# Kernel optimization log

Hardware: AMD Instinct MI355X
Metric: run time of the kernel (lower is better)

## Reference

```python
import jax, jax.numpy as jnp
import numpy as np

N_HEADS = 4
HEAD_DIM = 6
D_MODEL = 24


def setup_inputs() -> dict:
    key = jax.random.key(0)
    ks = jax.random.split(key, 7)
    B, Tq, Tk = 16, 1024, 1024
    X = jax.random.normal(ks[0], (B, Tq, D_MODEL), dtype=jnp.float32)
    X_en = jax.random.normal(ks[1], (B, Tk, D_MODEL), dtype=jnp.float32)
    I_m = jax.random.randint(ks[2], (B, Tq, Tk), 0, 2, dtype=jnp.int32)
    scale = 1.0 / np.sqrt(D_MODEL)
    Wq = jax.random.normal(ks[3], (D_MODEL, D_MODEL), dtype=jnp.float32) * scale
    Wk = jax.random.normal(ks[4], (D_MODEL, D_MODEL), dtype=jnp.float32) * scale
    Wv = jax.random.normal(ks[5], (D_MODEL, D_MODEL), dtype=jnp.float32) * scale
    Wo = jax.random.normal(ks[6], (D_MODEL, D_MODEL), dtype=jnp.float32) * scale
    return {"X": X, "X_en": X_en, "I_m": I_m, "Wq": Wq, "Wk": Wk, "Wv": Wv, "Wo": Wo}


def _split_heads(x):
    # [B, T, 24] -> [B, 4, T, 6]
    B, T, _ = x.shape
    return x.reshape(B, T, N_HEADS, HEAD_DIM).transpose(0, 2, 1, 3)


def reference(X, X_en, I_m, Wq, Wk, Wv, Wo):
    # torch Linear (no bias): x @ W.T
    Q = _split_heads(X @ Wq.T)      # [B, H, Tq, d]
    K = _split_heads(X_en @ Wk.T)   # [B, H, Tk, d]
    V = _split_heads(X_en @ Wv.T)   # [B, H, Tk, d]
    scale = 1.0 / jnp.sqrt(jnp.asarray(HEAD_DIM, dtype=Q.dtype))
    A = jnp.einsum('bhqd,bhkd->bhqk', Q, K) * scale
    # NOTE: the original torch code calls A.masked_fill(...) without assigning
    # the result, so the mask I_m has NO effect. Faithfully reproduced here.
    A = jax.nn.softmax(A, axis=-1)
    O = jnp.einsum('bhqk,bhkd->bhqd', A, V)  # [B, H, Tq, d]
    B, H, Tq, d = O.shape
    O = O.transpose(0, 2, 1, 3).reshape(B, Tq, H * d)  # [B, Tq, 24]
    return O @ Wo.T
```

## Files before the change

kernel.cpp:

```cpp
#include <hip/hip_runtime.h>
#include <hip/hip_bf16.h>

#define NB 16
#define TT 1024
#define NH 4
#define HD 6
#define DM 24

#define QSC 0.5889785f
#define MBIAS 32.0f

typedef float v2f __attribute__((ext_vector_type(2)));
typedef short bf16x8 __attribute__((ext_vector_type(8)));
typedef float f32x16 __attribute__((ext_vector_type(16)));
typedef unsigned u32x2 __attribute__((ext_vector_type(2)));

__device__ __forceinline__ unsigned cvt_pk_bf16(float lo, float hi) {
  unsigned r;
  asm("v_cvt_pk_bf16_f32 %0, %1, %2" : "=v"(r) : "v"(lo), "v"(hi));
  return r;
}

__device__ __forceinline__ bf16x8 as_bf16x8(uint4 u) {
  union { uint4 u; bf16x8 b; } c;
  c.u = u;
  return c.b;
}

__device__ __forceinline__ float dot24(const float4* r,
                                       const float* __restrict__ w) {
  v2f a = {0.f, 0.f};
#pragma unroll
  for (int i = 0; i < 6; ++i) {
    v2f xp, wp;
    xp.x = r[i].x; xp.y = r[i].y;
    wp.x = w[4 * i + 0]; wp.y = w[4 * i + 1];
    a = __builtin_elementwise_fma(xp, wp, a);
    xp.x = r[i].z; xp.y = r[i].w;
    wp.x = w[4 * i + 2]; wp.y = w[4 * i + 3];
    a = __builtin_elementwise_fma(xp, wp, a);
  }
  return a.x + a.y;
}

#define KSPLIT 2
#define KPB (TT / KSPLIT)
#define QB 128
#define ITERS (KPB / 32)

__global__ __launch_bounds__(256, 4) void fused_attn32_kernel(
    const float* __restrict__ X, const float* __restrict__ Xen,
    const float* __restrict__ Wq, const float* __restrict__ Wk,
    const float* __restrict__ Wv, float* __restrict__ P) {
  __shared__ __align__(16) uint4 Kl[KPB];
  __shared__ __align__(16) unsigned Vl[7][264];

  const int ks = blockIdx.x & 1;
  const int tile = (blockIdx.x >> 1) & 7;
  const int bh = blockIdx.x >> 4;
  const int b = bh >> 2, h = bh & 3;
  const int t = threadIdx.x;

  const float* __restrict__ wqh = Wq + h * HD * DM;
  const float* __restrict__ wkh = Wk + h * HD * DM;
  const float* __restrict__ wvh = Wv + h * HD * DM;

  {
    const float4* __restrict__ xe =
        (const float4*)(Xen + ((size_t)b * TT + ks * KPB + 2 * t) * DM);
    float4 xr[12];
#pragma unroll
    for (int i = 0; i < 12; ++i) xr[i] = xe[i];
    float kA[HD], kB[HD];
#pragma unroll
    for (int d = 0; d < HD; ++d) {
      kA[d] = dot24(xr + 0, wkh + d * DM);
      kB[d] = dot24(xr + 6, wkh + d * DM);
    }
    Kl[2 * t] = make_uint4(cvt_pk_bf16(kA[0], kA[1]), cvt_pk_bf16(kA[2], kA[3]),
                           cvt_pk_bf16(kA[4], kA[5]), 0u);
    Kl[2 * t + 1] =
        make_uint4(cvt_pk_bf16(kB[0], kB[1]), cvt_pk_bf16(kB[2], kB[3]),
                   cvt_pk_bf16(kB[4], kB[5]), 0u);
#pragma unroll
    for (int d = 0; d < HD; ++d) {
      const float vA = dot24(xr + 0, wvh + d * DM);
      const float vB = dot24(xr + 6, wvh + d * DM);
      Vl[d][t] = cvt_pk_bf16(vA, vB);
    }
    Vl[6][t] = 0x3F803F80u;
  }

  const int lane = t & 63;
  const int w = t >> 6;
  const int hi = lane >> 5;
  const int qc = lane & 31;
  const int q = tile * QB + w * 32 + qc;
  uint4 uq = make_uint4(0u, 0u, 0u, 0u);
  if (hi == 0) {
    const float4* __restrict__ xq =
        (const float4*)(X + ((size_t)b * TT + q) * DM);
    float4 xr[6];
#pragma unroll
    for (int i = 0; i < 6; ++i) xr[i] = xq[i];
    float qv[HD];
#pragma unroll
    for (int d = 0; d < HD; ++d) qv[d] = dot24(xr, wqh + d * DM) * QSC;
    uq = make_uint4(cvt_pk_bf16(qv[0], qv[1]), cvt_pk_bf16(qv[2], qv[3]),
                    cvt_pk_bf16(qv[4], qv[5]), 0u);
  }
  const bf16x8 qfrag = as_bf16x8(uq);

  __syncthreads();

  f32x16 cmb, oacc;
#pragma unroll
  for (int i = 0; i < 16; ++i) { cmb[i] = -MBIAS; oacc[i] = 0.f; }

  const int dcl = (qc < 7) ? qc : 6;
  const uint4 zero4 = make_uint4(0u, 0u, 0u, 0u);

#pragma unroll 2
  for (int it = 0; it < ITERS; ++it) {
    const uint4 ka = (hi == 0) ? Kl[it * 32 + qc] : zero4;
    const uint4 vv = *(const uint4*)&Vl[dcl][it * 16 + 4 * hi];

    f32x16 s = __builtin_amdgcn_mfma_f32_32x32x16_bf16(as_bf16x8(ka), qfrag,
                                                       cmb, 0, 0, 0);
    float p[16];
#pragma unroll
    for (int i = 0; i < 16; ++i) p[i] = __builtin_amdgcn_exp2f(s[i]);
    const unsigned c01 = cvt_pk_bf16(p[0], p[1]);
    const unsigned c23 = cvt_pk_bf16(p[2], p[3]);
    const unsigned c45 = cvt_pk_bf16(p[4], p[5]);
    const unsigned c67 = cvt_pk_bf16(p[6], p[7]);
    const unsigned c89 = cvt_pk_bf16(p[8], p[9]);
    const unsigned cAB = cvt_pk_bf16(p[10], p[11]);
    const unsigned cCD = cvt_pk_bf16(p[12], p[13]);
    const unsigned cEF = cvt_pk_bf16(p[14], p[15]);
    const u32x2 r0 = __builtin_amdgcn_permlane32_swap(c01, c45, false, false);
    const u32x2 r1 = __builtin_amdgcn_permlane32_swap(c23, c67, false, false);
    const u32x2 r2 = __builtin_amdgcn_permlane32_swap(c89, cCD, false, false);
    const u32x2 r3 = __builtin_amdgcn_permlane32_swap(cAB, cEF, false, false);
    const uint4 pb0 = make_uint4(r0[0], r1[0], r0[1], r1[1]);
    const uint4 pb1 = make_uint4(r2[0], r3[0], r2[1], r3[1]);
    oacc = __builtin_amdgcn_mfma_f32_32x32x16_bf16(as_bf16x8(vv),
                                                   as_bf16x8(pb0), oacc, 0, 0, 0);
    const uint4 vv2 = *(const uint4*)&Vl[dcl][it * 16 + 8 + 4 * hi];
    oacc = __builtin_amdgcn_mfma_f32_32x32x16_bf16(as_bf16x8(vv2),
                                                   as_bf16x8(pb1), oacc, 0, 0, 0);
  }

  const float a4 = __shfl_xor(oacc[0], 32);
  const float a5 = __shfl_xor(oacc[1], 32);
  const float ll = __shfl_xor(oacc[2], 32);
  if (hi == 0) {
    float* __restrict__ Pr = P + (((size_t)(bh * KSPLIT + ks)) * TT + q) * 8;
    ((float4*)Pr)[0] = make_float4(ll, oacc[0], oacc[1], oacc[2]);
    ((float4*)Pr)[1] = make_float4(oacc[3], a4, a5, 0.f);
  }
}

__global__ __launch_bounds__(256, 4) void combine_outproj_kernel(
    const float* __restrict__ P, const float* __restrict__ Wo,
    float* __restrict__ out) {
  __shared__ float wsh[DM * DM];
  __shared__ float o[32][25];
  for (int i = threadIdx.x; i < DM * DM; i += 256) wsh[i] = Wo[i];
  const int r0 = blockIdx.x * 32;
  {
    const int unit = threadIdx.x >> 1, e = threadIdx.x & 1;
    const int rl = unit >> 2, h = unit & 3;
    const int r = r0 + rl, b = r >> 10, t = r & (TT - 1);
    const int bh = b * NH + h;
    const float4* __restrict__ pp =
        (const float4*)(P + (((size_t)(bh * KSPLIT + e)) * TT + t) * 8);
    float4 x0 = pp[0], x1 = pp[1];
    float l = x0.x, a0 = x0.y, a1 = x0.z, a2 = x0.w;
    float a3 = x1.x, a4 = x1.y, a5 = x1.z;
    l += __shfl_xor(l, 1);
    a0 += __shfl_xor(a0, 1);
    a1 += __shfl_xor(a1, 1);
    a2 += __shfl_xor(a2, 1);
    a3 += __shfl_xor(a3, 1);
    a4 += __shfl_xor(a4, 1);
    a5 += __shfl_xor(a5, 1);
    if (e == 0) {
      const float inv = 1.f / l;
      o[rl][h * HD + 0] = a0 * inv;
      o[rl][h * HD + 1] = a1 * inv;
      o[rl][h * HD + 2] = a2 * inv;
      o[rl][h * HD + 3] = a3 * inv;
      o[rl][h * HD + 4] = a4 * inv;
      o[rl][h * HD + 5] = a5 * inv;
    }
  }
  __syncthreads();
  const int rl = threadIdx.x >> 3, u = threadIdx.x & 7;
  const int r = r0 + rl;
  float x[DM];
#pragma unroll
  for (int c = 0; c < DM; ++c) x[c] = o[rl][c];
#pragma unroll
  for (int jj = 0; jj < 3; ++jj) {
    const int j = u * 3 + jj;
    float a = 0.f;
#pragma unroll
    for (int c = 0; c < DM; ++c) a = fmaf(x[c], wsh[j * DM + c], a);
    out[(size_t)r * DM + j] = a;
  }
}

extern "C" void kernel_launch(void* const* d_in, const int* in_sizes, int n_in,
                              void* d_out, int out_size, void* d_ws, size_t ws_size,
                              hipStream_t stream) {
  const float* X = (const float*)d_in[0];
  const float* Xen = (const float*)d_in[1];
  const float* Wq = (const float*)d_in[3];
  const float* Wk = (const float*)d_in[4];
  const float* Wv = (const float*)d_in[5];
  const float* Wo = (const float*)d_in[6];

  float* P = (float*)d_ws;

  fused_attn32_kernel<<<NB * NH * 8 * KSPLIT, 256, 0, stream>>>(X, Xen, Wq,
                                                                Wk, Wv, P);
  combine_outproj_kernel<<<NB * TT / 32, 256, 0, stream>>>(P, Wo,
                                                           (float*)d_out);
}
```

Measured before the change: 25.00 us.

## Precompute K/V projections in a separate kernel instead of per attention block

Adds a kernel that projects X_en into bf16 K and transposed V once per (batch, head, key split) and stores them in the workspace. The attention kernel then loads these precomputed values into shared memory, where previously each of the 8 query tiles recomputed the same projection. This removes redundant projection arithmetic at the cost of an extra kernel launch and a global round trip for K/V.

```diff
diff --git a/kernel.cpp b/kernel.cpp
--- a/kernel.cpp
+++ b/kernel.cpp
@@ -25,6 +25,12 @@
   union { uint4 u; bf16x8 b; } c;
   c.u = u;
   return c.b;
+}
+
+__device__ __forceinline__ unsigned short bf16of(float v) {
+  union { __hip_bfloat16 b; unsigned short u; } c;
+  c.b = __float2bfloat16(v);
+  return c.u;
 }
 
 __device__ __forceinline__ float dot24(const float4* r,
@@ -48,10 +54,43 @@
 #define QB 128
 #define ITERS (KPB / 32)
 
+__global__ __launch_bounds__(256, 4) void kvproj_kernel(
+    const float* __restrict__ Xen, const float* __restrict__ Wk,
+    const float* __restrict__ Wv, uint4* __restrict__ Kg,
+    unsigned short* __restrict__ Vt) {
+  const int gid = blockIdx.x * 256 + threadIdx.x;
+  const int role = gid & 1;
+  const int kg = gid >> 1;
+  const int bh = kg >> 10;
+  const int key = kg & (TT - 1);
+  const int b = bh >> 2, h = bh & 3;
+  const int ks = key >> 9, loc = key & (KPB - 1);
+  const float* __restrict__ w =
+      (role ? Wv : Wk) + h * HD * DM;
+  const float4* __restrict__ xa =
+      (const float4*)(Xen + ((size_t)b * TT + key) * DM);
+  float4 xr[6];
+#pragma unroll
+  for (int i = 0; i < 6; ++i) xr[i] = xa[i];
+  float o[HD];
+#pragma unroll
+  for (int d = 0; d < HD; ++d) o[d] = dot24(xr, w + d * DM);
+  if (role == 0) {
+    Kg[((size_t)(bh * KSPLIT + ks)) * KPB + loc] =
+        make_uint4(cvt_pk_bf16(o[0], o[1]), cvt_pk_bf16(o[2], o[3]),
+                   cvt_pk_bf16(o[4], o[5]), 0u);
+  } else {
+    unsigned short* __restrict__ vt =
+        Vt + ((size_t)(bh * KSPLIT + ks)) * (7 * KPB);
+#pragma unroll
+    for (int d = 0; d < HD; ++d) vt[d * KPB + loc] = bf16of(o[d]);
+  }
+}
+
 __global__ __launch_bounds__(256, 4) void fused_attn32_kernel(
-    const float* __restrict__ X, const float* __restrict__ Xen,
-    const float* __restrict__ Wq, const float* __restrict__ Wk,
-    const float* __restrict__ Wv, float* __restrict__ P) {
+    const float* __restrict__ X, const float* __restrict__ Wq,
+    const uint4* __restrict__ Kg, const unsigned short* __restrict__ Vt,
+    float* __restrict__ P) {
   __shared__ __align__(16) uint4 Kl[KPB];
   __shared__ __align__(16) unsigned Vl[7][264];
 
@@ -61,41 +100,22 @@
   const int b = bh >> 2, h = bh & 3;
   const int t = threadIdx.x;
 
-  const float* __restrict__ wqh = Wq + h * HD * DM;
-  const float* __restrict__ wkh = Wk + h * HD * DM;
-  const float* __restrict__ wvh = Wv + h * HD * DM;
-
-  {
-    const float4* __restrict__ xe =
-        (const float4*)(Xen + ((size_t)b * TT + ks * KPB + 2 * t) * DM);
-    float4 xr[12];
-#pragma unroll
-    for (int i = 0; i < 12; ++i) xr[i] = xe[i];
-    float kA[HD], kB[HD];
-#pragma unroll
-    for (int d = 0; d < HD; ++d) {
-      kA[d] = dot24(xr + 0, wkh + d * DM);
-      kB[d] = dot24(xr + 6, wkh + d * DM);
-    }
-    Kl[2 * t] = make_uint4(cvt_pk_bf16(kA[0], kA[1]), cvt_pk_bf16(kA[2], kA[3]),
-                           cvt_pk_bf16(kA[4], kA[5]), 0u);
-    Kl[2 * t + 1] =
-        make_uint4(cvt_pk_bf16(kB[0], kB[1]), cvt_pk_bf16(kB[2], kB[3]),
-                   cvt_pk_bf16(kB[4], kB[5]), 0u);
-#pragma unroll
-    for (int d = 0; d < HD; ++d) {
-      const float vA = dot24(xr + 0, wvh + d * DM);
-      const float vB = dot24(xr + 6, wvh + d * DM);
-      Vl[d][t] = cvt_pk_bf16(vA, vB);
-    }
-    Vl[6][t] = 0x3F803F80u;
-  }
+  const uint4* __restrict__ Kgp = Kg + ((size_t)(bh * KSPLIT + ks)) * KPB;
+  const unsigned short* __restrict__ Vtp =
+      Vt + ((size_t)(bh * KSPLIT + ks)) * (7 * KPB);
+  const uint4 k0 = Kgp[2 * t];
+  const uint4 k1 = Kgp[2 * t + 1];
+  unsigned vr[HD];
+#pragma unroll
+  for (int d = 0; d < HD; ++d)
+    vr[d] = *(const unsigned*)(Vtp + d * KPB + 2 * t);
 
   const int lane = t & 63;
   const int w = t >> 6;
   const int hi = lane >> 5;
   const int qc = lane & 31;
   const int q = tile * QB + w * 32 + qc;
+  const float* __restrict__ wqh = Wq + h * HD * DM;
   uint4 uq = make_uint4(0u, 0u, 0u, 0u);
   if (hi == 0) {
     const float4* __restrict__ xq =
@@ -110,6 +130,12 @@
                     cvt_pk_bf16(qv[4], qv[5]), 0u);
   }
   const bf16x8 qfrag = as_bf16x8(uq);
+
+  Kl[2 * t] = k0;
+  Kl[2 * t + 1] = k1;
+#pragma unroll
+  for (int d = 0; d < HD; ++d) Vl[d][t] = vr[d];
+  Vl[6][t] = 0x3F803F80u;
 
   __syncthreads();
 
@@ -221,10 +247,16 @@
   const float* Wv = (const float*)d_in[5];
   const float* Wo = (const float*)d_in[6];
 
-  float* P = (float*)d_ws;
-
-  fused_attn32_kernel<<<NB * NH * 8 * KSPLIT, 256, 0, stream>>>(X, Xen, Wq,
-                                                                Wk, Wv, P);
+  char* ws = (char*)d_ws;
+  float* P = (float*)ws;
+  uint4* Kg = (uint4*)(ws + 4u * 1024 * 1024);
+  unsigned short* Vt =
+      (unsigned short*)(ws + 5u * 1024 * 1024);
+
+  kvproj_kernel<<<NB * NH * TT * 2 / 256, 256, 0, stream>>>(Xen, Wk, Wv, Kg,
+                                                            Vt);
+  fused_attn32_kernel<<<NB * NH * 8 * KSPLIT, 256, 0, stream>>>(X, Wq, Kg, Vt,
+                                                                P);
   combine_outproj_kernel<<<NB * TT / 32, 256, 0, stream>>>(P, Wo,
                                                            (float*)d_out);
 }
```

Result: slower. 28.43 us (+13.7%).

## Double query tile per block and split K/V projection across thread halves

Applied to the files above, without the earlier changes.

Each block now covers 256 queries with 512 threads instead of 128 queries with 256 threads, which halves the number of blocks and so halves how often the per-block K/V projection is recomputed. The K and V projections are split so one half of the threads computes K and the other half computes V, shortening the serial prologue per thread. The cost is a larger block, which may lower occupancy, and only 512 blocks to spread across the CUs.

```diff
diff --git a/kernel.cpp b/kernel.cpp
--- a/kernel.cpp
+++ b/kernel.cpp
@@ -45,10 +45,10 @@
 
 #define KSPLIT 2
 #define KPB (TT / KSPLIT)
-#define QB 128
+#define QB 256
 #define ITERS (KPB / 32)
 
-__global__ __launch_bounds__(256, 4) void fused_attn32_kernel(
+__global__ __launch_bounds__(512, 4) void fused_attn32_kernel(
     const float* __restrict__ X, const float* __restrict__ Xen,
     const float* __restrict__ Wq, const float* __restrict__ Wk,
     const float* __restrict__ Wv, float* __restrict__ P) {
@@ -56,10 +56,12 @@
   __shared__ __align__(16) unsigned Vl[7][264];
 
   const int ks = blockIdx.x & 1;
-  const int tile = (blockIdx.x >> 1) & 7;
-  const int bh = blockIdx.x >> 4;
+  const int tile = (blockIdx.x >> 1) & 3;
+  const int bh = blockIdx.x >> 3;
   const int b = bh >> 2, h = bh & 3;
   const int t = threadIdx.x;
+  const int pr = t & 255;
+  const int role = t >> 8;
 
   const float* __restrict__ wqh = Wq + h * HD * DM;
   const float* __restrict__ wkh = Wk + h * HD * DM;
@@ -67,28 +69,29 @@
 
   {
     const float4* __restrict__ xe =
-        (const float4*)(Xen + ((size_t)b * TT + ks * KPB + 2 * t) * DM);
+        (const float4*)(Xen + ((size_t)b * TT + ks * KPB + 2 * pr) * DM);
     float4 xr[12];
 #pragma unroll
     for (int i = 0; i < 12; ++i) xr[i] = xe[i];
-    float kA[HD], kB[HD];
+    const float* __restrict__ wr = role ? wvh : wkh;
+    float oA[HD], oB[HD];
 #pragma unroll
     for (int d = 0; d < HD; ++d) {
-      kA[d] = dot24(xr + 0, wkh + d * DM);
-      kB[d] = dot24(xr + 6, wkh + d * DM);
+      oA[d] = dot24(xr + 0, wr + d * DM);
+      oB[d] = dot24(xr + 6, wr + d * DM);
     }
-    Kl[2 * t] = make_uint4(cvt_pk_bf16(kA[0], kA[1]), cvt_pk_bf16(kA[2], kA[3]),
-                           cvt_pk_bf16(kA[4], kA[5]), 0u);
-    Kl[2 * t + 1] =
-        make_uint4(cvt_pk_bf16(kB[0], kB[1]), cvt_pk_bf16(kB[2], kB[3]),
-                   cvt_pk_bf16(kB[4], kB[5]), 0u);
-#pragma unroll
-    for (int d = 0; d < HD; ++d) {
-      const float vA = dot24(xr + 0, wvh + d * DM);
-      const float vB = dot24(xr + 6, wvh + d * DM);
-      Vl[d][t] = cvt_pk_bf16(vA, vB);
+    if (role == 0) {
+      Kl[2 * pr] =
+          make_uint4(cvt_pk_bf16(oA[0], oA[1]), cvt_pk_bf16(oA[2], oA[3]),
+                     cvt_pk_bf16(oA[4], oA[5]), 0u);
+      Kl[2 * pr + 1] =
+          make_uint4(cvt_pk_bf16(oB[0], oB[1]), cvt_pk_bf16(oB[2], oB[3]),
+                     cvt_pk_bf16(oB[4], oB[5]), 0u);
+    } else {
+#pragma unroll
+      for (int d = 0; d < HD; ++d) Vl[d][pr] = cvt_pk_bf16(oA[d], oB[d]);
+      Vl[6][pr] = 0x3F803F80u;
     }
-    Vl[6][t] = 0x3F803F80u;
   }
 
   const int lane = t & 63;
@@ -223,7 +226,7 @@
 
   float* P = (float*)d_ws;
 
-  fused_attn32_kernel<<<NB * NH * 8 * KSPLIT, 256, 0, stream>>>(X, Xen, Wq,
+  fused_attn32_kernel<<<NB * NH * 4 * KSPLIT, 512, 0, stream>>>(X, Xen, Wq,
                                                                 Wk, Wv, P);
   combine_outproj_kernel<<<NB * TT / 32, 256, 0, stream>>>(P, Wo,
                                                            (float*)d_out);
```

Result: slower. 28.27 us (+13.1%).
